# Kernel tuning notes

Measured on AMD Instinct MI355X. Metric: run time of the kernel, lower is better.

The kernel has to match this reference:

```python
import jax, jax.numpy as jnp
import numpy as np

B, S, C, M, L = 32, 8192, 64, 16, 4  # batch, seq, n_enc, n_modes, n_layers


def setup_inputs() -> dict:
    key = jax.random.key(0)
    ks = jax.random.split(key, 12)
    scale = 1.0 / (C * M)
    return {
        "input_tensor": jax.random.normal(ks[0], (B, S, 1), dtype=jnp.float32),
        "enc_w": jax.random.normal(ks[1], (C, 1), dtype=jnp.float32) * 0.1,
        "enc_b": jax.random.normal(ks[2], (C,), dtype=jnp.float32) * 0.1,
        "R_re": jax.random.normal(ks[3], (L, C, C, M), dtype=jnp.float32) * scale,
        "R_im": jax.random.normal(ks[4], (L, C, C, M), dtype=jnp.float32) * scale,
        "Wl_w": jax.random.normal(ks[5], (L, C, C), dtype=jnp.float32) * 0.1,
        "Wl_b": jax.random.normal(ks[6], (L, C), dtype=jnp.float32) * 0.1,
        "d1_w": jax.random.normal(ks[7], (C, C), dtype=jnp.float32) * 0.1,
        "d1_b": jax.random.normal(ks[8], (C,), dtype=jnp.float32) * 0.1,
        "d2_w": jax.random.normal(ks[9], (1, C), dtype=jnp.float32) * 0.1,
        "d2_b": jax.random.normal(ks[10], (1,), dtype=jnp.float32) * 0.1,
    }


def reference(input_tensor, enc_w, enc_b, R_re, R_im, Wl_w, Wl_b, d1_w, d1_b, d2_w, d2_b):
    # encoder: Conv1d(1, C, k=1) == per-position dense over channel dim
    h = jnp.einsum('bsi,ci->bsc', input_tensor, enc_w) + enc_b  # [B,S,C]
    n_freq = S // 2 + 1
    for l in range(L):
        x_cs = jnp.swapaxes(h, 1, 2)                 # [B,C,S]
        x_ft = jnp.fft.rfft(x_cs, axis=-1)           # [B,C,n_freq] complex
        Rl = R_re[l] + 1j * R_im[l]                  # [C,C,M]
        y = jnp.einsum('bim,iom->bom', x_ft[:, :, :M], Rl)  # [B,C,M]
        y_full = jnp.concatenate(
            [y, jnp.zeros((B, C, n_freq - M), dtype=y.dtype)], axis=-1)
        spat = jnp.fft.irfft(y_full, n=S, axis=-1)   # [B,C,S] float32
        wout = jnp.einsum('oi,bis->bos', Wl_w[l], x_cs) + Wl_b[l][None, :, None]
        h = jax.nn.gelu(jnp.swapaxes(spat + wout, 1, 2), approximate=False)
    z = jax.nn.gelu(jnp.einsum('bsc,oc->bso', h, d1_w) + d1_b, approximate=False)
    out = jnp.einsum('bso,po->bsp', z, d2_w) + d2_b  # [B,S,1]
    return out
```

## Files before the change

kernel.cpp:

```cpp
#include <hip/hip_runtime.h>
#include <math.h>

#define NB 32
#define NS 8192
#define NC 64
#define NM 16
#define NL 4
#define NM2 32
#define TPOS 128
#define NT (NS/TPOS)
#define PAD 65

typedef float f16v __attribute__((ext_vector_type(16)));
typedef float f4v  __attribute__((ext_vector_type(4)));

static __device__ __forceinline__ f4v zero4() {
    f4v v;
    #pragma unroll
    for (int j = 0; j < 4; ++j) v[j] = 0.0f;
    return v;
}

static __device__ __forceinline__ float gelu_exact(float v) {
    return 0.5f * v * (1.0f + erff(v * 0.7071067811865475f));
}

__global__ void k_table(float* __restrict__ T) {
    int s = blockIdx.x * blockDim.x + threadIdx.x;
    if (s >= NS) return;
    const float w = 6.283185307179586f / (float)NS;
    float* row = T + (size_t)s * NM2;
    #pragma unroll
    for (int m = 0; m < NM; ++m) {
        int idx = (m * s) & (NS - 1);
        float a = w * (float)idx;
        float sv, cv;
        sincosf(a, &sv, &cv);
        row[2*m]   = cv;
        row[2*m+1] = sv;
    }
}

__global__ void k_prep(const float* __restrict__ Ww, const float* __restrict__ d1w,
                       float* __restrict__ Wt, float* __restrict__ d1t) {
    int idx = blockIdx.x * 256 + threadIdx.x;
    if (idx < NL*NC*NC) {
        int l = idx / (NC*NC), r = idx % (NC*NC);
        int i = r / NC, o = r % NC;
        Wt[idx] = Ww[(size_t)l*NC*NC + (size_t)o*NC + i];
    } else if (idx < NL*NC*NC + NC*NC) {
        int r = idx - NL*NC*NC;
        int i = r / NC, o = r % NC;
        d1t[r] = d1w[(size_t)o*NC + i];
    }
}

static __device__ __forceinline__ void dft_phase(
        const float* __restrict__ hs, const float* __restrict__ T,
        float* __restrict__ partial, int b, int tile, int s0, int t) {
    int c  = t & 63;
    int kg = __builtin_amdgcn_readfirstlane(t >> 6);
    f4v acc = zero4();
    const float* trow = T + (size_t)s0 * NM2 + kg * 4;
    #pragma unroll 4
    for (int ss = 0; ss < TPOS; ++ss) {
        float hv = hs[ss * PAD + c];
        f4v tv = *(const f4v*)(trow + (size_t)ss * NM2);
        acc += hv * tv;
    }
    float* pout = partial + (((size_t)b*NT + tile)*NC + c)*NM2 + kg*4;
    *(f4v*)pout = acc;
}

__global__ void __launch_bounds__(512) k_enc(const float* __restrict__ x,
                                             const float* __restrict__ ew,
                                             const float* __restrict__ eb,
                                             const float* __restrict__ T,
                                             float* __restrict__ h,
                                             float* __restrict__ partial) {
    __shared__ float hs[TPOS * PAD];
    int tile = blockIdx.x, b = blockIdx.y;
    int t = threadIdx.x;
    int og = __builtin_amdgcn_readfirstlane(t >> 7);
    int p  = t & 127;
    int s0 = tile * TPOS;

    float xv = x[(size_t)b*NS + s0 + p];
    f16v ew16 = *(const f16v*)(ew + og*16);
    f16v eb16 = *(const f16v*)(eb + og*16);
    f16v hv = xv * ew16 + eb16;

    *(f16v*)(h + ((size_t)b*NS + s0 + p)*NC + og*16) = hv;

    #pragma unroll
    for (int j = 0; j < 16; ++j) hs[p*PAD + og*16 + j] = hv[j];
    __syncthreads();

    dft_phase(hs, T, partial, b, tile, s0, t);
}

__global__ void __launch_bounds__(256) k_mix(const float* __restrict__ partial,
                                             const float* __restrict__ Rre,
                                             const float* __restrict__ Rim,
                                             float* __restrict__ yst, int l) {
    __shared__ float xf[NC * 8];
    int b = blockIdx.x, jg = blockIdx.y, t = threadIdx.x;
    #pragma unroll
    for (int e = 0; e < 2; ++e) {
        int idx = t + 256*e;
        int c = idx >> 3, kk = idx & 7;
        const float* pp = partial + (size_t)b*NT*NC*NM2 + (size_t)c*NM2 + 8*jg + kk;
        float s = 0.f;
        #pragma unroll 8
        for (int tile = 0; tile < NT; ++tile)
            s += pp[(size_t)tile * NC * NM2];
        xf[idx] = s;
    }
    __syncthreads();
    {
        int o = t >> 2, mq = t & 3;
        int m = 4*jg + mq;
        float yre = 0.f, yim = 0.f;
        #pragma unroll 8
        for (int i = 0; i < NC; ++i) {
            float xr = xf[i*8 + 2*mq];
            float xs = xf[i*8 + 2*mq + 1];
            size_t ridx = (((size_t)l*NC + i)*NC + o)*NM + m;
            float rr = Rre[ridx], ri = Rim[ridx];
            yre = fmaf(xr, rr, yre); yre = fmaf(xs, ri, yre);
            yim = fmaf(xr, ri, yim); yim = fmaf(-xs, rr, yim);
        }
        float* yb = yst + (size_t)b*NM2*NC;
        if (m == 0) { yb[o] = yre * (1.0f/NS); yb[NC + o] = 0.f; }
        else {
            yb[(size_t)(2*m)*NC + o]   = yre * (2.0f/NS);
            yb[(size_t)(2*m+1)*NC + o] = -yim * (2.0f/NS);
        }
    }
}

template<bool LAST>
__global__ void __launch_bounds__(512) k_spec(float* __restrict__ h,
                                              const float* __restrict__ T,
                                              const float* __restrict__ yst,
                                              const float* __restrict__ Wt,
                                              const float* __restrict__ Wb,
                                              const float* __restrict__ d1t,
                                              const float* __restrict__ d1b,
                                              const float* __restrict__ d2w,
                                              const float* __restrict__ d2b,
                                              float* __restrict__ partial,
                                              float* __restrict__ outp,
                                              int l) {
    __shared__ float hs[TPOS * PAD];
    int tile = blockIdx.x, b = blockIdx.y;
    int t = threadIdx.x;
    int og = __builtin_amdgcn_readfirstlane(t >> 7);
    int p  = t & 127;
    int s0 = tile * TPOS;

    const float4* hblk = (const float4*)(h + ((size_t)b*NS + s0)*NC);
    float4 ld0 = hblk[t];
    float4 ld1 = hblk[t + 512];
    float4 ld2 = hblk[t + 1024];
    float4 ld3 = hblk[t + 1536];

    const float* Wl = Wt + (size_t)l*NC*NC + og*16;
    const float* bl = Wb + (size_t)l*NC + og*16;
    const float* yb = yst + (size_t)b*NM2*NC + og*16;

    f16v acc = *(const f16v*)bl;

    {
        acc += *(const f16v*)yb;
        float ang = (float)(s0 + p) * (6.283185307179586f / (float)NS);
        float c1, s1;
        sincosf(ang, &s1, &c1);
        float cm = c1, sm = s1;
        #pragma unroll 1
        for (int m = 1; m < NM; ++m) {
            f16v yc  = *(const f16v*)(yb + (size_t)(2*m)*NC);
            f16v ysv = *(const f16v*)(yb + (size_t)(2*m+1)*NC);
            acc += cm * yc;
            acc += sm * ysv;
            float cn = cm*c1 - sm*s1;
            sm = cm*s1 + sm*c1;
            cm = cn;
        }
    }

    {
        int ss = t >> 4, q4 = (t & 15) * 4;
        float* d;
        d = &hs[ss*PAD + q4];       d[0]=ld0.x; d[1]=ld0.y; d[2]=ld0.z; d[3]=ld0.w;
        d = &hs[(ss+32)*PAD + q4];  d[0]=ld1.x; d[1]=ld1.y; d[2]=ld1.z; d[3]=ld1.w;
        d = &hs[(ss+64)*PAD + q4];  d[0]=ld2.x; d[1]=ld2.y; d[2]=ld2.z; d[3]=ld2.w;
        d = &hs[(ss+96)*PAD + q4];  d[0]=ld3.x; d[1]=ld3.y; d[2]=ld3.z; d[3]=ld3.w;
    }
    __syncthreads();

    const float* hrow = &hs[p * PAD];
    #pragma unroll 8
    for (int i = 0; i < NC; ++i) {
        float hv = hrow[i];
        f16v w = *(const f16v*)(Wl + (size_t)i*NC);
        acc += hv * w;
    }

    f16v g;
    #pragma unroll
    for (int j = 0; j < 16; ++j) g[j] = gelu_exact(acc[j]);
    if (!LAST) {
        *(f16v*)(h + ((size_t)b*NS + s0 + p)*NC + og*16) = g;
    }

    __syncthreads();
    #pragma unroll
    for (int j = 0; j < 16; ++j) hs[p*PAD + og*16 + j] = g[j];
    __syncthreads();

    if (!LAST) {
        dft_phase(hs, T, partial, b, tile, s0, t);
    } else {
        f16v a = *(const f16v*)(d1b + og*16);
        const float* hr = &hs[p * PAD];
        #pragma unroll 8
        for (int i = 0; i < NC; ++i) {
            float hv = hr[i];
            f16v w = *(const f16v*)(d1t + (size_t)i*NC + og*16);
            a += hv * w;
        }
        float res = 0.f;
        #pragma unroll
        for (int j = 0; j < 16; ++j)
            res = fmaf(gelu_exact(a[j]), d2w[og*16 + j], res);
        __syncthreads();
        hs[og*TPOS + p] = res;
        __syncthreads();
        if (t < TPOS) {
            outp[(size_t)b*NS + s0 + t] = d2b[0] + hs[t] + hs[TPOS + t]
                                        + hs[2*TPOS + t] + hs[3*TPOS + t];
        }
    }
}

extern "C" void kernel_launch(void* const* d_in, const int* in_sizes, int n_in,
                              void* d_out, int out_size, void* d_ws, size_t ws_size,
                              hipStream_t stream) {
    const float* input = (const float*)d_in[0];
    const float* enc_w = (const float*)d_in[1];
    const float* enc_b = (const float*)d_in[2];
    const float* R_re  = (const float*)d_in[3];
    const float* R_im  = (const float*)d_in[4];
    const float* Wl_w  = (const float*)d_in[5];
    const float* Wl_b  = (const float*)d_in[6];
    const float* d1_w  = (const float*)d_in[7];
    const float* d1_b  = (const float*)d_in[8];
    const float* d2_w  = (const float*)d_in[9];
    const float* d2_b  = (const float*)d_in[10];
    float* out = (float*)d_out;

    float* ws  = (float*)d_ws;
    float* h   = ws;
    float* T   = h   + (size_t)NB*NS*NC;
    float* par = T   + (size_t)NS*NM2;
    float* yst = par + (size_t)NB*NT*NC*NM2;
    float* Wt  = yst + (size_t)NB*NM2*NC;
    float* d1t = Wt  + (size_t)NL*NC*NC;

    hipLaunchKernelGGL(k_table, dim3(NS/256), dim3(256), 0, stream, T);
    hipLaunchKernelGGL(k_prep, dim3((NL*NC*NC + NC*NC + 255)/256), dim3(256), 0,
                       stream, Wl_w, d1_w, Wt, d1t);
    hipLaunchKernelGGL(k_enc, dim3(NT, NB), dim3(512), 0, stream,
                       input, enc_w, enc_b, T, h, par);
    for (int l = 0; l < NL; ++l) {
        hipLaunchKernelGGL(k_mix, dim3(NB, 4), dim3(256), 0, stream,
                           par, R_re, R_im, yst, l);
        if (l < NL - 1) {
            hipLaunchKernelGGL((k_spec<false>), dim3(NT, NB), dim3(512), 0, stream,
                               h, T, yst, Wt, Wl_b, d1t, d1_b, d2_w, d2_b,
                               par, out, l);
        } else {
            hipLaunchKernelGGL((k_spec<true>), dim3(NT, NB), dim3(512), 0, stream,
                               h, T, yst, Wt, Wl_b, d1t, d1_b, d2_w, d2_b,
                               par, out, l);
        }
    }
}
```

Before: 372.7 us.

## Move spectral layer matmuls and DFT onto bf16 MFMA with split hi/lo precision

```diff
diff --git a/kernel.cpp b/kernel.cpp
--- a/kernel.cpp
+++ b/kernel.cpp
@@ -10,44 +10,67 @@
 #define TPOS 128
 #define NT (NS/TPOS)
 #define PAD 65
-
-typedef float f16v __attribute__((ext_vector_type(16)));
-typedef float f4v  __attribute__((ext_vector_type(4)));
-
-static __device__ __forceinline__ f4v zero4() {
-    f4v v;
-    #pragma unroll
-    for (int j = 0; j < 4; ++j) v[j] = 0.0f;
-    return v;
-}
-
+#define APAD 68
+#define GPAD 132
+
+typedef float f16v  __attribute__((ext_vector_type(16)));
+typedef float f4v   __attribute__((ext_vector_type(4)));
+typedef short bf16x8 __attribute__((ext_vector_type(8)));
+typedef short bf16x4 __attribute__((ext_vector_type(4)));
+
+#define MFMA16(a,b,c) __builtin_amdgcn_mfma_f32_16x16x32_bf16(a,b,c,0,0,0)
+
+static __device__ __forceinline__ unsigned short f2bf(float x) {
+    unsigned u = __float_as_uint(x);
+    u += 0x7FFFu + ((u >> 16) & 1u);
+    return (unsigned short)(u >> 16);
+}
+static __device__ __forceinline__ float bf2f(unsigned short b) {
+    return __uint_as_float(((unsigned)b) << 16);
+}
+static __device__ __forceinline__ bf16x8 ld8l(const unsigned short* p) {
+    bf16x4 a = *(const bf16x4*)p;
+    bf16x4 b = *(const bf16x4*)(p + 4);
+    return __builtin_shufflevector(a, b, 0, 1, 2, 3, 4, 5, 6, 7);
+}
 static __device__ __forceinline__ float gelu_exact(float v) {
     return 0.5f * v * (1.0f + erff(v * 0.7071067811865475f));
 }
 
-__global__ void k_table(float* __restrict__ T) {
-    int s = blockIdx.x * blockDim.x + threadIdx.x;
+__global__ void k_table(float* __restrict__ T,
+                        unsigned short* __restrict__ Thi,
+                        unsigned short* __restrict__ Tlo,
+                        unsigned short* __restrict__ TThi,
+                        unsigned short* __restrict__ TTlo) {
+    int s = blockIdx.x * 256 + threadIdx.x;
     if (s >= NS) return;
     const float w = 6.283185307179586f / (float)NS;
-    float* row = T + (size_t)s * NM2;
     #pragma unroll
     for (int m = 0; m < NM; ++m) {
         int idx = (m * s) & (NS - 1);
-        float a = w * (float)idx;
         float sv, cv;
-        sincosf(a, &sv, &cv);
-        row[2*m]   = cv;
-        row[2*m+1] = sv;
+        sincosf(w * (float)idx, &sv, &cv);
+        T[(size_t)s*NM2 + 2*m]   = cv;
+        T[(size_t)s*NM2 + 2*m+1] = sv;
+        unsigned short ch = f2bf(cv), cl = f2bf(cv - bf2f(f2bf(cv)));
+        unsigned short sh = f2bf(sv), sl = f2bf(sv - bf2f(f2bf(sv)));
+        Thi[(size_t)s*NM2 + 2*m]   = ch;  Tlo[(size_t)s*NM2 + 2*m]   = cl;
+        Thi[(size_t)s*NM2 + 2*m+1] = sh;  Tlo[(size_t)s*NM2 + 2*m+1] = sl;
+        TThi[(size_t)(2*m)*NS + s]   = ch;  TTlo[(size_t)(2*m)*NS + s]   = cl;
+        TThi[(size_t)(2*m+1)*NS + s] = sh;  TTlo[(size_t)(2*m+1)*NS + s] = sl;
     }
 }
 
 __global__ void k_prep(const float* __restrict__ Ww, const float* __restrict__ d1w,
-                       float* __restrict__ Wt, float* __restrict__ d1t) {
+                       unsigned short* __restrict__ Wbhi,
+                       unsigned short* __restrict__ Wblo,
+                       float* __restrict__ d1t) {
     int idx = blockIdx.x * 256 + threadIdx.x;
     if (idx < NL*NC*NC) {
-        int l = idx / (NC*NC), r = idx % (NC*NC);
-        int i = r / NC, o = r % NC;
-        Wt[idx] = Ww[(size_t)l*NC*NC + (size_t)o*NC + i];
+        float v = Ww[idx];
+        unsigned short hi = f2bf(v);
+        Wbhi[idx] = hi;
+        Wblo[idx] = f2bf(v - bf2f(hi));
     } else if (idx < NL*NC*NC + NC*NC) {
         int r = idx - NL*NC*NC;
         int i = r / NC, o = r % NC;
@@ -60,7 +83,7 @@
         float* __restrict__ partial, int b, int tile, int s0, int t) {
     int c  = t & 63;
     int kg = __builtin_amdgcn_readfirstlane(t >> 6);
-    f4v acc = zero4();
+    f4v acc = {0.f, 0.f, 0.f, 0.f};
     const float* trow = T + (size_t)s0 * NM2 + kg * 4;
     #pragma unroll 4
     for (int ss = 0; ss < TPOS; ++ss) {
@@ -102,7 +125,9 @@
 __global__ void __launch_bounds__(256) k_mix(const float* __restrict__ partial,
                                              const float* __restrict__ Rre,
                                              const float* __restrict__ Rim,
-                                             float* __restrict__ yst, int l) {
+                                             unsigned short* __restrict__ ysbThi,
+                                             unsigned short* __restrict__ ysbTlo,
+                                             int l) {
     __shared__ float xf[NC * 8];
     int b = blockIdx.x, jg = blockIdx.y, t = threadIdx.x;
     #pragma unroll
@@ -130,21 +155,28 @@
             yre = fmaf(xr, rr, yre); yre = fmaf(xs, ri, yre);
             yim = fmaf(xr, ri, yim); yim = fmaf(-xs, rr, yim);
         }
-        float* yb = yst + (size_t)b*NM2*NC;
-        if (m == 0) { yb[o] = yre * (1.0f/NS); yb[NC + o] = 0.f; }
-        else {
-            yb[(size_t)(2*m)*NC + o]   = yre * (2.0f/NS);
-            yb[(size_t)(2*m+1)*NC + o] = -yim * (2.0f/NS);
-        }
+        float v0, v1;
+        if (m == 0) { v0 = yre * (1.0f/NS); v1 = 0.f; }
+        else        { v0 = yre * (2.0f/NS); v1 = -yim * (2.0f/NS); }
+        size_t yb = ((size_t)b*NC + o)*NM2;
+        unsigned short h0 = f2bf(v0);
+        ysbThi[yb + 2*m]   = h0;  ysbTlo[yb + 2*m]   = f2bf(v0 - bf2f(h0));
+        unsigned short h1 = f2bf(v1);
+        ysbThi[yb + 2*m+1] = h1;  ysbTlo[yb + 2*m+1] = f2bf(v1 - bf2f(h1));
     }
 }
 
 template<bool LAST>
 __global__ void __launch_bounds__(512) k_spec(float* __restrict__ h,
-                                              const float* __restrict__ T,
-                                              const float* __restrict__ yst,
-                                              const float* __restrict__ Wt,
-                                              const float* __restrict__ Wb,
+                                              const unsigned short* __restrict__ Thi,
+                                              const unsigned short* __restrict__ Tlo,
+                                              const unsigned short* __restrict__ TThi,
+                                              const unsigned short* __restrict__ TTlo,
+                                              const unsigned short* __restrict__ ysbThi,
+                                              const unsigned short* __restrict__ ysbTlo,
+                                              const unsigned short* __restrict__ Wbhi,
+                                              const unsigned short* __restrict__ Wblo,
+                                              const float* __restrict__ Wlb,
                                               const float* __restrict__ d1t,
                                               const float* __restrict__ d1b,
                                               const float* __restrict__ d2w,
@@ -152,94 +184,158 @@
                                               float* __restrict__ partial,
                                               float* __restrict__ outp,
                                               int l) {
-    __shared__ float hs[TPOS * PAD];
+    __shared__ __align__(16) unsigned short uLDS[2 * TPOS * APAD];
+    unsigned short* hsAhi = uLDS;
+    unsigned short* hsAlo = uLDS + TPOS * APAD;
+
     int tile = blockIdx.x, b = blockIdx.y;
     int t = threadIdx.x;
-    int og = __builtin_amdgcn_readfirstlane(t >> 7);
-    int p  = t & 127;
+    int lane = t & 63, w = t >> 6;
+    int lm = lane & 15, g = lane >> 4;
     int s0 = tile * TPOS;
 
     const float4* hblk = (const float4*)(h + ((size_t)b*NS + s0)*NC);
-    float4 ld0 = hblk[t];
-    float4 ld1 = hblk[t + 512];
-    float4 ld2 = hblk[t + 1024];
-    float4 ld3 = hblk[t + 1536];
-
-    const float* Wl = Wt + (size_t)l*NC*NC + og*16;
-    const float* bl = Wb + (size_t)l*NC + og*16;
-    const float* yb = yst + (size_t)b*NM2*NC + og*16;
-
-    f16v acc = *(const f16v*)bl;
-
-    {
-        acc += *(const f16v*)yb;
-        float ang = (float)(s0 + p) * (6.283185307179586f / (float)NS);
-        float c1, s1;
-        sincosf(ang, &s1, &c1);
-        float cm = c1, sm = s1;
-        #pragma unroll 1
-        for (int m = 1; m < NM; ++m) {
-            f16v yc  = *(const f16v*)(yb + (size_t)(2*m)*NC);
-            f16v ysv = *(const f16v*)(yb + (size_t)(2*m+1)*NC);
-            acc += cm * yc;
-            acc += sm * ysv;
-            float cn = cm*c1 - sm*s1;
-            sm = cm*s1 + sm*c1;
-            cm = cn;
-        }
-    }
-
-    {
-        int ss = t >> 4, q4 = (t & 15) * 4;
-        float* d;
-        d = &hs[ss*PAD + q4];       d[0]=ld0.x; d[1]=ld0.y; d[2]=ld0.z; d[3]=ld0.w;
-        d = &hs[(ss+32)*PAD + q4];  d[0]=ld1.x; d[1]=ld1.y; d[2]=ld1.z; d[3]=ld1.w;
-        d = &hs[(ss+64)*PAD + q4];  d[0]=ld2.x; d[1]=ld2.y; d[2]=ld2.z; d[3]=ld2.w;
-        d = &hs[(ss+96)*PAD + q4];  d[0]=ld3.x; d[1]=ld3.y; d[2]=ld3.z; d[3]=ld3.w;
+    #pragma unroll
+    for (int j = 0; j < 4; ++j) {
+        float4 v = hblk[t + 512*j];
+        int idx = t + 512*j;
+        int pos = idx >> 4, q4 = (idx & 15) * 4;
+        float vv[4] = {v.x, v.y, v.z, v.w};
+        bf16x4 hi4, lo4;
+        #pragma unroll
+        for (int e = 0; e < 4; ++e) {
+            unsigned short hh = f2bf(vv[e]);
+            hi4[e] = (short)hh;
+            lo4[e] = (short)f2bf(vv[e] - bf2f(hh));
+        }
+        *(bf16x4*)(&hsAhi[pos*APAD + q4]) = hi4;
+        *(bf16x4*)(&hsAlo[pos*APAD + q4]) = lo4;
     }
     __syncthreads();
 
-    const float* hrow = &hs[p * PAD];
-    #pragma unroll 8
-    for (int i = 0; i < NC; ++i) {
-        float hv = hrow[i];
-        f16v w = *(const f16v*)(Wl + (size_t)i*NC);
-        acc += hv * w;
-    }
-
-    f16v g;
-    #pragma unroll
-    for (int j = 0; j < 16; ++j) g[j] = gelu_exact(acc[j]);
+    bf16x8 aHi[2], aLo[2];
+    #pragma unroll
+    for (int k2 = 0; k2 < 2; ++k2) {
+        int eo = (w*16 + lm)*APAD + k2*32 + 8*g;
+        aHi[k2] = ld8l(&hsAhi[eo]);
+        aLo[k2] = ld8l(&hsAlo[eo]);
+    }
+    bf16x8 tHi = *(const bf16x8*)(Thi + (size_t)(s0 + w*16 + lm)*NM2 + 8*g);
+    bf16x8 tLo = *(const bf16x8*)(Tlo + (size_t)(s0 + w*16 + lm)*NM2 + 8*g);
+
+    f4v acc[4];
+    #pragma unroll
+    for (int N = 0; N < 4; ++N) {
+        float bv = Wlb[(size_t)l*NC + N*16 + lm];
+        acc[N] = (f4v){bv, bv, bv, bv};
+    }
+
+    #pragma unroll
+    for (int N = 0; N < 4; ++N) {
+        size_t yo = ((size_t)b*NC + N*16 + lm)*NM2 + 8*g;
+        bf16x8 yHi = *(const bf16x8*)(ysbThi + yo);
+        bf16x8 yLo = *(const bf16x8*)(ysbTlo + yo);
+        acc[N] = MFMA16(tHi, yHi, acc[N]);
+        acc[N] = MFMA16(tHi, yLo, acc[N]);
+        acc[N] = MFMA16(tLo, yHi, acc[N]);
+    }
+
+    #pragma unroll
+    for (int k2 = 0; k2 < 2; ++k2) {
+        #pragma unroll
+        for (int N = 0; N < 4; ++N) {
+            size_t wo = ((size_t)l*NC + N*16 + lm)*NC + k2*32 + 8*g;
+            bf16x8 wHi = *(const bf16x8*)(Wbhi + wo);
+            bf16x8 wLo = *(const bf16x8*)(Wblo + wo);
+            acc[N] = MFMA16(aHi[k2], wHi, acc[N]);
+            acc[N] = MFMA16(aHi[k2], wLo, acc[N]);
+            acc[N] = MFMA16(aLo[k2], wHi, acc[N]);
+        }
+    }
+
+    f4v gv[4];
+    #pragma unroll
+    for (int N = 0; N < 4; ++N)
+        #pragma unroll
+        for (int r = 0; r < 4; ++r)
+            gv[N][r] = gelu_exact(acc[N][r]);
+
     if (!LAST) {
-        *(f16v*)(h + ((size_t)b*NS + s0 + p)*NC + og*16) = g;
+        #pragma unroll
+        for (int N = 0; N < 4; ++N)
+            #pragma unroll
+            for (int r = 0; r < 4; ++r)
+                h[((size_t)b*NS + s0 + w*16 + g*4 + r)*NC + N*16 + lm] = gv[N][r];
     }
 
     __syncthreads();
-    #pragma unroll
-    for (int j = 0; j < 16; ++j) hs[p*PAD + og*16 + j] = g[j];
-    __syncthreads();
 
     if (!LAST) {
-        dft_phase(hs, T, partial, b, tile, s0, t);
+        unsigned short* gThi = uLDS;
+        unsigned short* gTlo = uLDS + NC * GPAD;
+        #pragma unroll
+        for (int N = 0; N < 4; ++N) {
+            int c = N*16 + lm;
+            #pragma unroll
+            for (int r = 0; r < 4; ++r) {
+                int pos = w*16 + g*4 + r;
+                float v = gv[N][r];
+                unsigned short hh = f2bf(v);
+                gThi[c*GPAD + pos] = hh;
+                gTlo[c*GPAD + pos] = f2bf(v - bf2f(hh));
+            }
+        }
+        __syncthreads();
+
+        int Mblk = w & 3, Nblk = w >> 2;
+        f4v pacc = {0.f, 0.f, 0.f, 0.f};
+        #pragma unroll
+        for (int ks = 0; ks < 4; ++ks) {
+            int eo = (Mblk*16 + lm)*GPAD + ks*32 + 8*g;
+            bf16x8 gHi = ld8l(&gThi[eo]);
+            bf16x8 gLo = ld8l(&gTlo[eo]);
+            size_t to = (size_t)(Nblk*16 + lm)*NS + s0 + ks*32 + 8*g;
+            bf16x8 tbHi = *(const bf16x8*)(TThi + to);
+            bf16x8 tbLo = *(const bf16x8*)(TTlo + to);
+            pacc = MFMA16(gHi, tbHi, pacc);
+            pacc = MFMA16(gHi, tbLo, pacc);
+            pacc = MFMA16(gLo, tbHi, pacc);
+        }
+        float* pout = partial + ((size_t)b*NT + tile)*NC*NM2;
+        #pragma unroll
+        for (int r = 0; r < 4; ++r) {
+            int c = Mblk*16 + g*4 + r;
+            pout[(size_t)c*NM2 + Nblk*16 + lm] = pacc[r];
+        }
     } else {
-        f16v a = *(const f16v*)(d1b + og*16);
-        const float* hr = &hs[p * PAD];
+        float* hsf = (float*)uLDS;
+        #pragma unroll
+        for (int N = 0; N < 4; ++N)
+            #pragma unroll
+            for (int r = 0; r < 4; ++r)
+                hsf[(w*16 + g*4 + r)*PAD + N*16 + lm] = gv[N][r];
+        __syncthreads();
+
+        int og2 = __builtin_amdgcn_readfirstlane(t >> 7);
+        int p2  = t & 127;
+        f16v a = *(const f16v*)(d1b + og2*16);
+        const float* hr = hsf + p2*PAD;
         #pragma unroll 8
         for (int i = 0; i < NC; ++i) {
             float hv = hr[i];
-            f16v w = *(const f16v*)(d1t + (size_t)i*NC + og*16);
-            a += hv * w;
+            f16v wv = *(const f16v*)(d1t + (size_t)i*NC + og2*16);
+            a += hv * wv;
         }
         float res = 0.f;
         #pragma unroll
         for (int j = 0; j < 16; ++j)
-            res = fmaf(gelu_exact(a[j]), d2w[og*16 + j], res);
+            res = fmaf(gelu_exact(a[j]), d2w[og2*16 + j], res);
         __syncthreads();
-        hs[og*TPOS + p] = res;
+        hsf[og2*TPOS + p2] = res;
         __syncthreads();
         if (t < TPOS) {
-            outp[(size_t)b*NS + s0 + t] = d2b[0] + hs[t] + hs[TPOS + t]
-                                        + hs[2*TPOS + t] + hs[3*TPOS + t];
+            outp[(size_t)b*NS + s0 + t] = d2b[0] + hsf[t] + hsf[TPOS + t]
+                                        + hsf[2*TPOS + t] + hsf[3*TPOS + t];
         }
     }
 }
@@ -264,25 +360,34 @@
     float* h   = ws;
     float* T   = h   + (size_t)NB*NS*NC;
     float* par = T   + (size_t)NS*NM2;
-    float* yst = par + (size_t)NB*NT*NC*NM2;
-    float* Wt  = yst + (size_t)NB*NM2*NC;
-    float* d1t = Wt  + (size_t)NL*NC*NC;
-
-    hipLaunchKernelGGL(k_table, dim3(NS/256), dim3(256), 0, stream, T);
+    float* d1t = par + (size_t)NB*NT*NC*NM2;
+    unsigned short* Thi    = (unsigned short*)(d1t + NC*NC);
+    unsigned short* Tlo    = Thi    + (size_t)NS*NM2;
+    unsigned short* TThi   = Tlo    + (size_t)NS*NM2;
+    unsigned short* TTlo   = TThi   + (size_t)NM2*NS;
+    unsigned short* ysbThi = TTlo   + (size_t)NM2*NS;
+    unsigned short* ysbTlo = ysbThi + (size_t)NB*NC*NM2;
+    unsigned short* Wbhi   = ysbTlo + (size_t)NB*NC*NM2;
+    unsigned short* Wblo   = Wbhi   + (size_t)NL*NC*NC;
+
+    hipLaunchKernelGGL(k_table, dim3(NS/256), dim3(256), 0, stream,
+                       T, Thi, Tlo, TThi, TTlo);
     hipLaunchKernelGGL(k_prep, dim3((NL*NC*NC + NC*NC + 255)/256), dim3(256), 0,
-                       stream, Wl_w, d1_w, Wt, d1t);
+                       stream, Wl_w, d1_w, Wbhi, Wblo, d1t);
     hipLaunchKernelGGL(k_enc, dim3(NT, NB), dim3(512), 0, stream,
                        input, enc_w, enc_b, T, h, par);
     for (int l = 0; l < NL; ++l) {
         hipLaunchKernelGGL(k_mix, dim3(NB, 4), dim3(256), 0, stream,
-                           par, R_re, R_im, yst, l);
+                           par, R_re, R_im, ysbThi, ysbTlo, l);
         if (l < NL - 1) {
             hipLaunchKernelGGL((k_spec<false>), dim3(NT, NB), dim3(512), 0, stream,
-                               h, T, yst, Wt, Wl_b, d1t, d1_b, d2_w, d2_b,
+                               h, Thi, Tlo, TThi, TTlo, ysbThi, ysbTlo,
+                               Wbhi, Wblo, Wl_b, d1t, d1_b, d2_w, d2_b,
                                par, out, l);
         } else {
             hipLaunchKernelGGL((k_spec<true>), dim3(NT, NB), dim3(512), 0, stream,
-                               h, T, yst, Wt, Wl_b, d1t, d1_b, d2_w, d2_b,
+                               h, Thi, Tlo, TThi, TTlo, ysbThi, ysbTlo,
+                               Wbhi, Wblo, Wl_b, d1t, d1_b, d2_w, d2_b,
                                par, out, l);
         }
     }
```

Result: faster. 360.7 us (-3.2%).
